# Kernel tuning notes

Hardware: AMD Instinct MI355X
Metric: run time of the kernel (lower is better)

## Reference

```python
import jax, jax.numpy as jnp
import numpy as np

# J6 incidence matrix for Plucker coordinates (constant buffer in the torch module)
_J6 = jnp.array([[0, 0, 0, 0, 0, 1],
                 [0, 0, 0, 0, -1, 0],
                 [0, 0, 0, 1, 0, 0],
                 [0, 0, 1, 0, 0, 0],
                 [0, -1, 0, 0, 0, 0],
                 [1, 0, 0, 0, 0, 0]], dtype=jnp.float32)

# combinations(range(4), 2) index pairs for the exterior product
_PI = np.array([0, 0, 0, 1, 1, 2])
_PJ = np.array([1, 2, 3, 2, 3, 3])


def plucker_lines(p1, p2):
    # p1, p2: (..., 4) -> normalized Plucker 6-vectors (..., 6)
    lines = p1[..., _PI] * p2[..., _PJ] - p1[..., _PJ] * p2[..., _PI]
    n = jnp.linalg.norm(lines, axis=-1, keepdims=True)
    return lines / jnp.maximum(n, 1e-12)


def setup_inputs() -> dict:
    key = jax.random.key(0)
    ks = jax.random.split(key, 6)
    B, T, D, H = 1, 2048, 1024, 16
    s = D ** -0.5
    x = jax.random.normal(ks[0], (B, T, D), jnp.float32)
    Wqkv = jax.random.normal(ks[1], (D, 3 * D), jnp.float32) * s
    bqkv = jnp.zeros((3 * D,), jnp.float32)
    W1p = jax.random.normal(ks[2], (D, 4 * H), jnp.float32) * s
    W2p = jax.random.normal(ks[3], (D, 4 * H), jnp.float32) * s
    plucker_scale = jnp.full((H,), 0.1, jnp.float32)
    Wout = jax.random.normal(ks[4], (D, D), jnp.float32) * s
    bout = jnp.zeros((D,), jnp.float32)
    return {"x": x, "Wqkv": Wqkv, "bqkv": bqkv, "W1p": W1p, "W2p": W2p,
            "plucker_scale": plucker_scale, "Wout": Wout, "bout": bout}


def reference(x, Wqkv, bqkv, W1p, W2p, plucker_scale, Wout, bout):
    B, T, D = x.shape
    H = plucker_scale.shape[0]
    dh = D // H

    qkv = (x @ Wqkv + bqkv).reshape(B, T, 3, H, dh)
    q = jnp.transpose(qkv[:, :, 0], (0, 2, 1, 3))  # [B,H,T,dh]
    k = jnp.transpose(qkv[:, :, 1], (0, 2, 1, 3))
    v = jnp.transpose(qkv[:, :, 2], (0, 2, 1, 3))

    std_logits = jnp.einsum('bhid,bhjd->bhij', q, k) * (dh ** -0.5)

    p1 = (x @ W1p).reshape(B, T, H, 4)
    p2 = (x @ W2p).reshape(B, T, H, 4)
    lines_h = jnp.transpose(plucker_lines(p1, p2), (0, 2, 1, 3))  # [B,H,T,6]
    Jlines = lines_h @ _J6.T                                       # [B,H,T,6]
    plucker_bias = jnp.einsum('bhic,bhjc->bhij', lines_h, Jlines)  # [B,H,T,T]

    logits = std_logits + plucker_bias * plucker_scale[None, :, None, None]
    causal = jnp.triu(jnp.ones((T, T), bool), 1)
    logits = jnp.where(causal[None, None], -jnp.inf, logits)
    attn = jax.nn.softmax(logits, axis=-1)

    out = jnp.einsum('bhij,bhjd->bhid', attn, v)
    out = jnp.transpose(out, (0, 2, 1, 3)).reshape(B, T, D)
    return out @ Wout + bout
```

## Files before the change

kernel.cpp:

```cpp
#include <hip/hip_runtime.h>

typedef unsigned short u16;
typedef unsigned int u32;
typedef __attribute__((ext_vector_type(8))) __bf16 bf16x8;
typedef __attribute__((ext_vector_type(4))) float f32x4;
typedef __attribute__((ext_vector_type(4))) u16 u16x4;

#define MFMA16(a, b, c) __builtin_amdgcn_mfma_f32_16x16x32_bf16((a), (b), (c), 0, 0, 0)

static __device__ __forceinline__ u16 f2b(float f) {
  union { float f; u32 u; } v; v.f = f;
  u32 u = v.u;
  return (u16)((u + 0x7FFFu + ((u >> 16) & 1u)) >> 16);
}

static __device__ __forceinline__ u32 pack2(float a, float b) {
  u32 r;
  asm("v_cvt_pk_bf16_f32 %0, %1, %2" : "=v"(r) : "v"(a), "v"(b));
  return r;
}

static __device__ __forceinline__ float exp2fast(float x) {
#if defined(__has_builtin) && __has_builtin(__builtin_amdgcn_exp2f)
  return __builtin_amdgcn_exp2f(x);
#else
  return __expf(x * 0.6931471805599453f);
#endif
}

static __device__ __forceinline__ void gload16(const u16* gp, u16* lp) {
  __builtin_amdgcn_global_load_lds((__attribute__((address_space(1))) void*)(u16*)gp,
                                   (__attribute__((address_space(3))) void*)lp, 16, 0, 0);
}

__global__ __launch_bounds__(256) void k_prep(const float* __restrict__ Wqkv, const float* __restrict__ Wout,
                                              const float* __restrict__ W1p, const float* __restrict__ W2p,
                                              const float* __restrict__ x,
                                              u16* __restrict__ WB, u16* __restrict__ WoT,
                                              u16* __restrict__ xb) {
  const int b = blockIdx.x;
  const int t = threadIdx.x;
  if (b < 1024) {
    __shared__ float tile[64][65];
    const float* src; u16* dst; int N, n0, k0;
    if (b < 768) { src = Wqkv; dst = WB;  N = 3072; n0 = (b % 48) * 64; k0 = (b / 48) * 64; }
    else { const int bb = b - 768; src = Wout; dst = WoT; N = 1024; n0 = (bb & 15) * 64; k0 = (bb >> 4) * 64; }
    const int rr = t >> 4, cc = (t & 15) << 2;
#pragma unroll
    for (int i = 0; i < 4; ++i) {
      const float4 v = *(const float4*)(src + (size_t)(k0 + rr + i * 16) * N + n0 + cc);
      tile[rr + i * 16][cc + 0] = v.x; tile[rr + i * 16][cc + 1] = v.y;
      tile[rr + i * 16][cc + 2] = v.z; tile[rr + i * 16][cc + 3] = v.w;
    }
    __syncthreads();
    const int nr = t >> 3, kc = (t & 7) << 3;
#pragma unroll
    for (int i = 0; i < 2; ++i) {
      u16 o[8];
#pragma unroll
      for (int j = 0; j < 8; ++j) o[j] = f2b(tile[kc + j][nr + i * 32]);
      *(uint4*)(dst + (size_t)(n0 + nr + i * 32) * 1024 + k0 + kc) = *(const uint4*)o;
    }
  } else if (b < 1536) {
    const int idx = (b - 1024) * 256 + t;
    const int j = idx >> 10, k = idx & 1023;
    const float v = (j < 64) ? W1p[(size_t)k * 64 + j] : W2p[(size_t)k * 64 + (j - 64)];
    WB[(size_t)3072 * 1024 + idx] = f2b(v);
  } else {
    const size_t idx = ((size_t)(b - 1536) * 256 + t) << 2;
    const float4 v = *(const float4*)(x + idx);
    u16x4 o; o.x = f2b(v.x); o.y = f2b(v.y); o.z = f2b(v.z); o.w = f2b(v.w);
    *(u16x4*)(xb + idx) = o;
  }
}

static __device__ __forceinline__ void gemm_core_128x64(const u16* __restrict__ A, const u16* __restrict__ B,
                                                        int brow, int bcol, int K,
                                                        u16* ldsA, u16* ldsB, f32x4 acc[4][2]) {
  const int tid = threadIdx.x;
  const int wave = tid >> 6, lane = tid & 63;
  const int wr = wave >> 1, wc = wave & 1;
  const int g = lane >> 4, l15 = lane & 15;

  for (int k0 = 0; k0 < K; k0 += 64) {
#pragma unroll
    for (int li = 0; li < 4; ++li) {
      const int f = li * 256 + wave * 64 + lane;
      const int row = f >> 3;
      const int slot = f & 7;
      const int gcol = ((slot ^ (row & 7)) << 3);
      gload16(A + (size_t)(brow + row) * K + k0 + gcol, ldsA + (size_t)(li * 256 + wave * 64) * 8);
    }
#pragma unroll
    for (int li = 0; li < 2; ++li) {
      const int f = li * 256 + wave * 64 + lane;
      const int row = f >> 3;
      const int slot = f & 7;
      const int gcol = ((slot ^ (row & 7)) << 3);
      gload16(B + (size_t)(bcol + row) * K + k0 + gcol, ldsB + (size_t)(li * 256 + wave * 64) * 8);
    }
    __syncthreads();
    bf16x8 af[4][2], bfr[2][2];
#pragma unroll
    for (int kk = 0; kk < 2; ++kk) {
#pragma unroll
      for (int m = 0; m < 4; ++m) {
        const int rowA = wr * 64 + m * 16 + l15;
        const int chA = (kk * 4 + g) ^ (rowA & 7);
        af[m][kk] = *(const bf16x8*)(ldsA + (size_t)rowA * 64 + chA * 8);
      }
#pragma unroll
      for (int n = 0; n < 2; ++n) {
        const int rowB = wc * 32 + n * 16 + l15;
        const int chB = (kk * 4 + g) ^ (rowB & 7);
        bfr[n][kk] = *(const bf16x8*)(ldsB + (size_t)rowB * 64 + chB * 8);
      }
    }
#pragma unroll
    for (int m = 0; m < 4; ++m)
#pragma unroll
      for (int n = 0; n < 2; ++n)
#pragma unroll
        for (int kk = 0; kk < 2; ++kk)
          acc[m][n] = MFMA16(af[m][kk], bfr[n][kk], acc[m][n]);
    __syncthreads();
  }
}

__global__ __launch_bounds__(256) void k_gemm_qkvp(const u16* __restrict__ xb, const u16* __restrict__ WB,
                                                   const float* __restrict__ bqkv,
                                                   u16* __restrict__ Qext, u16* __restrict__ Kext,
                                                   u16* __restrict__ Vt, float* __restrict__ P12) {
  __shared__ __align__(16) u16 ldsA[128 * 64];
  __shared__ __align__(16) u16 ldsB[64 * 64];
  const int bid = blockIdx.x;
  const int bn = bid % 50, bm = bid / 50;
  f32x4 acc[4][2];
#pragma unroll
  for (int m = 0; m < 4; ++m)
#pragma unroll
    for (int n = 0; n < 2; ++n) acc[m][n] = (f32x4){0.f, 0.f, 0.f, 0.f};
  gemm_core_128x64(xb, WB, bm * 128, bn * 64, 1024, ldsA, ldsB, acc);

  const int tid = threadIdx.x;
  const int wave = tid >> 6, lane = tid & 63;
  const int wr = wave >> 1, wc = wave & 1;
  const int g = lane >> 4, l15 = lane & 15;
  const int tbase = bm * 128 + wr * 64 + g * 4;
  const int cbase = bn * 64 + wc * 32 + l15;
#pragma unroll
  for (int m = 0; m < 4; ++m) {
#pragma unroll
    for (int n = 0; n < 2; ++n) {
      const int c = cbase + n * 16;
#pragma unroll
      for (int r = 0; r < 4; ++r) {
        const int t = tbase + m * 16 + r;
        float v = acc[m][n][r];
        if (c < 3072) {
          v += bqkv[c];
          const int sub = c >> 10;
          const int rem = c & 1023;
          const int hh = rem >> 6, d = rem & 63;
          if (sub == 0)      Qext[((size_t)hh * 2048 + t) * 96 + d] = f2b(v * 0.18033688f);
          else if (sub == 1) Kext[((size_t)hh * 2048 + t) * 96 + d] = f2b(v);
          else               Vt[(size_t)hh * 131072 + (size_t)(t >> 5) * 2048 + d * 32 + (t & 31)] = f2b(v);
        } else {
          P12[(size_t)t * 128 + (c - 3072)] = v;
        }
      }
    }
  }
}

__global__ __launch_bounds__(256) void k_lines(const float* __restrict__ P12, const float* __restrict__ pscale,
                                               u16* __restrict__ Qext, u16* __restrict__ Kext) {
  const int idx = blockIdx.x * 256 + threadIdx.x;
  const int t = idx >> 4, h = idx & 15;
  const float* p = P12 + (size_t)t * 128;
  const float a0 = p[h * 4 + 0], a1 = p[h * 4 + 1], a2 = p[h * 4 + 2], a3 = p[h * 4 + 3];
  const float b0 = p[64 + h * 4 + 0], b1 = p[64 + h * 4 + 1], b2 = p[64 + h * 4 + 2], b3 = p[64 + h * 4 + 3];
  float L0 = a0 * b1 - a1 * b0;
  float L1 = a0 * b2 - a2 * b0;
  float L2 = a0 * b3 - a3 * b0;
  float L3 = a1 * b2 - a2 * b1;
  float L4 = a1 * b3 - a3 * b1;
  float L5 = a2 * b3 - a3 * b2;
  const float nrm = sqrtf(L0 * L0 + L1 * L1 + L2 * L2 + L3 * L3 + L4 * L4 + L5 * L5);
  const float inv = 1.0f / fmaxf(nrm, 1e-12f);
  L0 *= inv; L1 *= inv; L2 *= inv; L3 *= inv; L4 *= inv; L5 *= inv;
  const float s = pscale[h] * 1.44269504f;
  u16* q = Qext + ((size_t)h * 2048 + t) * 96 + 64;
  u16* k = Kext + ((size_t)h * 2048 + t) * 96 + 64;
  q[0] = f2b(L0 * s); q[1] = f2b(L1 * s); q[2] = f2b(L2 * s);
  q[3] = f2b(L3 * s); q[4] = f2b(L4 * s); q[5] = f2b(L5 * s);
  k[0] = f2b(L5); k[1] = f2b(-L4); k[2] = f2b(L3);
  k[3] = f2b(L2); k[4] = f2b(-L1); k[5] = f2b(L0);
#pragma unroll
  for (int c = 6; c < 32; ++c) { q[c] = 0; k[c] = 0; }
}

__global__ __launch_bounds__(128) void k_attn(const u16* __restrict__ Qext, const u16* __restrict__ Kext,
                                              const u16* __restrict__ Vt, u16* __restrict__ AO) {
  const int bid = blockIdx.x;
  const int h = bid & 15;
  const int p = ((bid >> 4) << 1) + (threadIdx.x >> 6);
  const int lane = threadIdx.x & 63;
  const int g = lane >> 4, l15 = lane & 15;
  const int q0A = p << 4;
  const int q0B = (127 - p) << 4;
  const int qgA = q0A + l15;
  const int qgB = q0B + l15;
  const int sA = (p >> 1) + 1;
  const int sB = ((127 - p) >> 1) + 1;
  const u16* Qh = Qext + (size_t)h * 2048 * 96;
  const u16* Kh = Kext + (size_t)h * 2048 * 96;
  const u16* Vh = Vt + (size_t)h * 131072;

  bf16x8 aqA[3], aqB[3];
#pragma unroll
  for (int ks = 0; ks < 3; ++ks) {
    aqA[ks] = *(const bf16x8*)(Qh + (size_t)qgA * 96 + ks * 32 + g * 8);
    aqB[ks] = *(const bf16x8*)(Qh + (size_t)qgB * 96 + ks * 32 + g * 8);
  }

  f32x4 accA[4], accB[4];
#pragma unroll
  for (int n = 0; n < 4; ++n) {
    accA[n] = (f32x4){0.f, 0.f, 0.f, 0.f};
    accB[n] = (f32x4){0.f, 0.f, 0.f, 0.f};
  }
  float lA = 0.f, lB = 0.f;

  const u16* Kbase = Kh + (size_t)l15 * 96 + g * 8;
  const u16* Vlane = Vh + (size_t)l15 * 32 + g * 8;

  bf16x8 kX0[3], kX1[3], kY0[3], kY1[3];
  bf16x8 avX[4], avY[4];
  f32x4 SA0c, SA1c, SB0c, SB1c, SA0n, SA1n, SB0n, SB1n;

  {
#pragma unroll
    for (int ks = 0; ks < 3; ++ks) {
      kX0[ks] = *(const bf16x8*)(Kbase + ks * 32);
      kX1[ks] = *(const bf16x8*)(Kbase + 16 * 96 + ks * 32);
    }
    SB0c = (f32x4){0.f, 0.f, 0.f, 0.f}; SB1c = SB0c; SA0c = SB0c; SA1c = SB0c;
#pragma unroll
    for (int ks = 0; ks < 3; ++ks) {
      SB0c = MFMA16(kX0[ks], aqB[ks], SB0c);
      SB1c = MFMA16(kX1[ks], aqB[ks], SB1c);
      SA0c = MFMA16(kX0[ks], aqA[ks], SA0c);
      SA1c = MFMA16(kX1[ks], aqA[ks], SA1c);
    }
    const u16* kp = Kbase + (size_t)((1 < sB) ? 1 : 0) * 32 * 96;
#pragma unroll
    for (int ks = 0; ks < 3; ++ks) {
      kY0[ks] = *(const bf16x8*)(kp + ks * 32);
      kY1[ks] = *(const bf16x8*)(kp + 16 * 96 + ks * 32);
    }
#pragma unroll
    for (int n = 0; n < 4; ++n) avX[n] = *(const bf16x8*)(Vlane + n * 512);
  }

#define GLUE(S0, S1, Q0S, QGS, LS, PBS)                                           \
  {                                                                               \
    if (jb + 31 > Q0S) {                                                          \
      _Pragma("unroll")                                                           \
      for (int r = 0; r < 4; ++r) {                                               \
        if (jb + g * 4 + r > QGS) S0[r] = -1e30f;                                 \
        if (jb + 16 + g * 4 + r > QGS) S1[r] = -1e30f;                            \
      }                                                                           \
    }                                                                             \
    _Pragma("unroll")                                                             \
    for (int r = 0; r < 4; ++r) {                                                 \
      S0[r] = exp2fast(S0[r]);                                                    \
      S1[r] = exp2fast(S1[r]);                                                    \
    }                                                                             \
    LS += ((S0[0] + S0[1]) + (S0[2] + S0[3])) + ((S1[0] + S1[1]) + (S1[2] + S1[3])); \
    u32 a0 = pack2(S0[0], S0[1]);                                                 \
    u32 a1 = pack2(S0[2], S0[3]);                                                 \
    u32 b0 = pack2(S1[0], S1[1]);                                                 \
    u32 b1 = pack2(S1[2], S1[3]);                                                 \
    asm("v_permlane32_swap_b32 %0, %1" : "+v"(a0), "+v"(b0));                     \
    asm("v_permlane16_swap_b32 %0, %1" : "+v"(a0), "+v"(b0));                     \
    asm("v_permlane32_swap_b32 %0, %1" : "+v"(a1), "+v"(b1));                     \
    asm("v_permlane16_swap_b32 %0, %1" : "+v"(a1), "+v"(b1));                     \
    PBS.u[0] = a0;                                                                \
    PBS.u[1] = a1;                                                                \
    PBS.u[2] = b0;                                                                \
    PBS.u[3] = b1;                                                                \
  }

#define ATTN_STEP(SA0C, SA1C, SB0C, SB1C, SA0N, SA1N, SB0N, SB1N, KN0, KN1, KL0, KL1, AVC, AVN) \
  {                                                                               \
    const int jb = jt * 32;                                                       \
    const int jn1 = (jt + 1 < sB) ? jt + 1 : jt;                                  \
    const int jn2 = (jt + 2 < sB) ? jt + 2 : jt;                                  \
                                     \
    SB0N = (f32x4){0.f, 0.f, 0.f, 0.f}; SB1N = SB0N;                              \
    __builtin_amdgcn_s_setprio(1);                                                \
    _Pragma("unroll")                                                             \
    for (int ks = 0; ks < 3; ++ks) {                                              \
      SB0N = MFMA16(KN0[ks], aqB[ks], SB0N);                                      \
      SB1N = MFMA16(KN1[ks], aqB[ks], SB1N);                                      \
    }                                                                             \
    if (jt + 1 < sA) {                                                            \
      SA0N = (f32x4){0.f, 0.f, 0.f, 0.f}; SA1N = SA0N;                            \
      _Pragma("unroll")                                                           \
      for (int ks = 0; ks < 3; ++ks) {                                            \
        SA0N = MFMA16(KN0[ks], aqA[ks], SA0N);                                    \
        SA1N = MFMA16(KN1[ks], aqA[ks], SA1N);                                    \
      }                                                                           \
    }                                                                             \
    __builtin_amdgcn_s_setprio(0);                                                \
                                                         \
    const u16* kp = Kbase + (size_t)jn2 * 32 * 96;                                \
    _Pragma("unroll")                                                             \
    for (int ks = 0; ks < 3; ++ks) {                                              \
      KL0[ks] = *(const bf16x8*)(kp + ks * 32);                                   \
      KL1[ks] = *(const bf16x8*)(kp + 16 * 96 + ks * 32);                         \
    }                                                                             \
                                                         \
    _Pragma("unroll")                                                             \
    for (int n = 0; n < 4; ++n)                                                   \
      AVN[n] = *(const bf16x8*)(Vlane + (size_t)jn1 * 2048 + n * 512);            \
                                                      \
    union { u32 u[4]; bf16x8 bv; } pbB, pbA;                                      \
    GLUE(SB0C, SB1C, q0B, qgB, lB, pbB);                                          \
    const bool actA = (jt < sA);                                                  \
    if (actA) GLUE(SA0C, SA1C, q0A, qgA, lA, pbA);                                \
                                                 \
    __builtin_amdgcn_s_setprio(1);                                                \
    _Pragma("unroll")                                                             \
    for (int n = 0; n < 4; ++n) accB[n] = MFMA16(AVC[n], pbB.bv, accB[n]);        \
    if (actA) {                                                                   \
      _Pragma("unroll")                                                           \
      for (int n = 0; n < 4; ++n) accA[n] = MFMA16(AVC[n], pbA.bv, accA[n]);      \
    }                                                                             \
    __builtin_amdgcn_s_setprio(0);                                                \
  }

  int jt = 0;
  for (;;) {
    ATTN_STEP(SA0c, SA1c, SB0c, SB1c, SA0n, SA1n, SB0n, SB1n, kY0, kY1, kX0, kX1, avX, avY);
    if (++jt >= sB) break;
    ATTN_STEP(SA0n, SA1n, SB0n, SB1n, SA0c, SA1c, SB0c, SB1c, kX0, kX1, kY0, kY1, avY, avX);
    if (++jt >= sB) break;
  }
#undef ATTN_STEP
#undef GLUE

  lA += __shfl_xor(lA, 16);
  lA += __shfl_xor(lA, 32);
  lB += __shfl_xor(lB, 16);
  lB += __shfl_xor(lB, 32);
  const float invA = 1.0f / lA;
  const float invB = 1.0f / lB;
  u32* dstA = (u32*)(AO + (size_t)qgA * 1024 + h * 64 + g * 4);
  u32* dstB = (u32*)(AO + (size_t)qgB * 1024 + h * 64 + g * 4);
#pragma unroll
  for (int n = 0; n < 4; ++n) {
    dstA[n * 8 + 0] = pack2(accA[n][0] * invA, accA[n][1] * invA);
    dstA[n * 8 + 1] = pack2(accA[n][2] * invA, accA[n][3] * invA);
    dstB[n * 8 + 0] = pack2(accB[n][0] * invB, accB[n][1] * invB);
    dstB[n * 8 + 1] = pack2(accB[n][2] * invB, accB[n][3] * invB);
  }
}

__global__ __launch_bounds__(256) void k_gemm_out(const u16* __restrict__ AO, const u16* __restrict__ WoT,
                                                  const float* __restrict__ bout, float* __restrict__ out) {
  __shared__ __align__(16) u16 ldsA[128 * 64];
  __shared__ __align__(16) u16 ldsB[32 * 64];
  const int bid = blockIdx.x;
  const int bn = bid & 31, bm = bid >> 5;
  const int tid = threadIdx.x;
  const int wave = tid >> 6, lane = tid & 63;
  const int wr = wave >> 1, wc = wave & 1;
  const int g = lane >> 4, l15 = lane & 15;

  f32x4 acc[4];
#pragma unroll
  for (int m = 0; m < 4; ++m) acc[m] = (f32x4){0.f, 0.f, 0.f, 0.f};

  for (int k0 = 0; k0 < 1024; k0 += 64) {
#pragma unroll
    for (int li = 0; li < 4; ++li) {
      const int f = li * 256 + wave * 64 + lane;
      const int row = f >> 3;
      const int slot = f & 7;
      const int gcol = ((slot ^ (row & 7)) << 3);
      gload16(AO + (size_t)(bm * 128 + row) * 1024 + k0 + gcol, ldsA + (size_t)(li * 256 + wave * 64) * 8);
    }
    {
      const int f = wave * 64 + lane;
      const int row = f >> 3;
      const int slot = f & 7;
      const int gcol = ((slot ^ (row & 7)) << 3);
      gload16(WoT + (size_t)(bn * 32 + row) * 1024 + k0 + gcol, ldsB + (size_t)(wave * 64) * 8);
    }
    __syncthreads();
    bf16x8 af[4][2], bfr[2];
#pragma unroll
    for (int kk = 0; kk < 2; ++kk) {
#pragma unroll
      for (int m = 0; m < 4; ++m) {
        const int rowA = wr * 64 + m * 16 + l15;
        const int chA = (kk * 4 + g) ^ (rowA & 7);
        af[m][kk] = *(const bf16x8*)(ldsA + (size_t)rowA * 64 + chA * 8);
      }
      const int rowB = wc * 16 + l15;
      const int chB = (kk * 4 + g) ^ (rowB & 7);
      bfr[kk] = *(const bf16x8*)(ldsB + (size_t)rowB * 64 + chB * 8);
    }
#pragma unroll
    for (int m = 0; m < 4; ++m)
#pragma unroll
      for (int kk = 0; kk < 2; ++kk)
        acc[m] = MFMA16(af[m][kk], bfr[kk], acc[m]);
    __syncthreads();
  }

  const int tbase = bm * 128 + wr * 64 + g * 4;
  const int c = bn * 32 + wc * 16 + l15;
  const float bb = bout[c];
#pragma unroll
  for (int m = 0; m < 4; ++m)
#pragma unroll
    for (int r = 0; r < 4; ++r) {
      const int t = tbase + m * 16 + r;
      out[(size_t)t * 1024 + c] = acc[m][r] + bb;
    }
}

extern "C" void kernel_launch(void* const* d_in, const int* in_sizes, int n_in,
                              void* d_out, int out_size, void* d_ws, size_t ws_size,
                              hipStream_t stream) {
  const float* x      = (const float*)d_in[0];
  const float* Wqkv   = (const float*)d_in[1];
  const float* bqkv   = (const float*)d_in[2];
  const float* W1p    = (const float*)d_in[3];
  const float* W2p    = (const float*)d_in[4];
  const float* pscale = (const float*)d_in[5];
  const float* Wout   = (const float*)d_in[6];
  const float* bout   = (const float*)d_in[7];
  float* out = (float*)d_out;

  char* ws = (char*)d_ws;
  u16*   WB    = (u16*)(ws + 0);
  u16*   WoT   = (u16*)(ws + 6553600);
  u16*   xb    = (u16*)(ws + 8650752);
  u16*   Qext  = (u16*)(ws + 12845056);
  u16*   Kext  = (u16*)(ws + 19136512);
  u16*   Vt    = (u16*)(ws + 25427968);
  float* P12   = (float*)(ws + 29622272);
  u16*   AO    = (u16*)(ws + 30670848);

  k_prep<<<3584, 256, 0, stream>>>(Wqkv, Wout, W1p, W2p, x, WB, WoT, xb);
  k_gemm_qkvp<<<800, 256, 0, stream>>>(xb, WB, bqkv, Qext, Kext, Vt, P12);
  k_lines<<<128, 256, 0, stream>>>(P12, pscale, Qext, Kext);
  k_attn<<<512, 128, 0, stream>>>(Qext, Kext, Vt, AO);
  k_gemm_out<<<512, 256, 0, stream>>>(AO, WoT, bout, out);
}
```

Before: 98.92 us.

## Share K/V tiles across four waves via double-buffered LDS in attention

Attention blocks now hold four waves covering 64 consecutive queries of one head. They cooperatively stage each 32-key K/V tile into a double-buffered LDS region, instead of every wave streaming K/V from global memory on its own. K is written by the QKV GEMM and the lines kernel in a pre-swizzled MFMA-fragment layout, so each stage is a contiguous copy and each wave reads its fragment with one vector load per chunk. This cuts redundant global/L2 K/V traffic. In exchange it drops the old two-query-tile interleaving that balanced causal work and hid latency, and adds a block barrier per key tile, where waves with shorter causal ranges sit idle.

```diff
diff --git a/kernel.cpp b/kernel.cpp
--- a/kernel.cpp
+++ b/kernel.cpp
@@ -129,7 +129,7 @@
 
 __global__ __launch_bounds__(256) void k_gemm_qkvp(const u16* __restrict__ xb, const u16* __restrict__ WB,
                                                    const float* __restrict__ bqkv,
-                                                   u16* __restrict__ Qext, u16* __restrict__ Kext,
+                                                   u16* __restrict__ Qext, u16* __restrict__ Kf,
                                                    u16* __restrict__ Vt, float* __restrict__ P12) {
   __shared__ __align__(16) u16 ldsA[128 * 64];
   __shared__ __align__(16) u16 ldsB[64 * 64];
@@ -162,9 +162,15 @@
           const int sub = c >> 10;
           const int rem = c & 1023;
           const int hh = rem >> 6, d = rem & 63;
-          if (sub == 0)      Qext[((size_t)hh * 2048 + t) * 96 + d] = f2b(v * 0.18033688f);
-          else if (sub == 1) Kext[((size_t)hh * 2048 + t) * 96 + d] = f2b(v);
-          else               Vt[(size_t)hh * 131072 + (size_t)(t >> 5) * 2048 + d * 32 + (t & 31)] = f2b(v);
+          if (sub == 0) {
+            Qext[((size_t)hh * 2048 + t) * 96 + d] = f2b(v * 0.18033688f);
+          } else if (sub == 1) {
+            const int jt2 = t >> 5, hf = (t >> 4) & 1, l15t = t & 15;
+            const int ks2 = d >> 5, gg = (d >> 3) & 3, e = d & 7;
+            Kf[(size_t)hh * 196608 + (size_t)jt2 * 3072 + (hf * 3 + ks2) * 512 + (gg * 16 + l15t) * 8 + e] = f2b(v);
+          } else {
+            Vt[(size_t)hh * 131072 + (size_t)(t >> 5) * 2048 + d * 32 + (t & 31)] = f2b(v);
+          }
         } else {
           P12[(size_t)t * 128 + (c - 3072)] = v;
         }
@@ -174,7 +180,7 @@
 }
 
 __global__ __launch_bounds__(256) void k_lines(const float* __restrict__ P12, const float* __restrict__ pscale,
-                                               u16* __restrict__ Qext, u16* __restrict__ Kext) {
+                                               u16* __restrict__ Qext, u16* __restrict__ Kf) {
   const int idx = blockIdx.x * 256 + threadIdx.x;
   const int t = idx >> 4, h = idx & 15;
   const float* p = P12 + (size_t)t * 128;
@@ -191,180 +197,129 @@
   L0 *= inv; L1 *= inv; L2 *= inv; L3 *= inv; L4 *= inv; L5 *= inv;
   const float s = pscale[h] * 1.44269504f;
   u16* q = Qext + ((size_t)h * 2048 + t) * 96 + 64;
-  u16* k = Kext + ((size_t)h * 2048 + t) * 96 + 64;
   q[0] = f2b(L0 * s); q[1] = f2b(L1 * s); q[2] = f2b(L2 * s);
   q[3] = f2b(L3 * s); q[4] = f2b(L4 * s); q[5] = f2b(L5 * s);
-  k[0] = f2b(L5); k[1] = f2b(-L4); k[2] = f2b(L3);
-  k[3] = f2b(L2); k[4] = f2b(-L1); k[5] = f2b(L0);
-#pragma unroll
-  for (int c = 6; c < 32; ++c) { q[c] = 0; k[c] = 0; }
-}
-
-__global__ __launch_bounds__(128) void k_attn(const u16* __restrict__ Qext, const u16* __restrict__ Kext,
+#pragma unroll
+  for (int c = 6; c < 32; ++c) q[c] = 0;
+  const float kv0 = L5, kv1 = -L4, kv2 = L3, kv3 = L2, kv4 = -L1, kv5 = L0;
+  const int jt = t >> 5, hf = (t >> 4) & 1, l15t = t & 15;
+  u16* kf = Kf + (size_t)h * 196608 + (size_t)jt * 3072 + (hf * 3 + 2) * 512;
+#pragma unroll
+  for (int j = 0; j < 32; ++j) {
+    const int gg = (j >> 3) & 3, e = j & 7;
+    float val;
+    if (j == 0) val = kv0; else if (j == 1) val = kv1; else if (j == 2) val = kv2;
+    else if (j == 3) val = kv3; else if (j == 4) val = kv4; else if (j == 5) val = kv5;
+    else val = 0.f;
+    kf[(gg * 16 + l15t) * 8 + e] = (j < 6) ? f2b(val) : (u16)0;
+  }
+}
+
+__global__ __launch_bounds__(256) void k_attn(const u16* __restrict__ Qext, const u16* __restrict__ Kf,
                                               const u16* __restrict__ Vt, u16* __restrict__ AO) {
-  const int bid = blockIdx.x;
-  const int h = bid & 15;
-  const int p = ((bid >> 4) << 1) + (threadIdx.x >> 6);
-  const int lane = threadIdx.x & 63;
+  __shared__ __align__(16) u16 KV[2][5120];
+  const int idx = blockIdx.x;
+  const int half = idx >> 8;
+  const int qt_raw = (idx & 255) >> 4;
+  const int qt = half ? (31 - qt_raw) : qt_raw;
+  const int h = idx & 15;
+  const int wave = threadIdx.x >> 6, lane = threadIdx.x & 63;
   const int g = lane >> 4, l15 = lane & 15;
-  const int q0A = p << 4;
-  const int q0B = (127 - p) << 4;
-  const int qgA = q0A + l15;
-  const int qgB = q0B + l15;
-  const int sA = (p >> 1) + 1;
-  const int sB = ((127 - p) >> 1) + 1;
+  const int q0 = qt * 64 + wave * 16;
+  const int q_glob = q0 + l15;
+  const int sW = (q0 >> 5) + 1;
+  const int sBlk = qt * 2 + 2;
   const u16* Qh = Qext + (size_t)h * 2048 * 96;
-  const u16* Kh = Kext + (size_t)h * 2048 * 96;
-  const u16* Vh = Vt + (size_t)h * 131072;
-
-  bf16x8 aqA[3], aqB[3];
-#pragma unroll
-  for (int ks = 0; ks < 3; ++ks) {
-    aqA[ks] = *(const bf16x8*)(Qh + (size_t)qgA * 96 + ks * 32 + g * 8);
-    aqB[ks] = *(const bf16x8*)(Qh + (size_t)qgB * 96 + ks * 32 + g * 8);
-  }
-
-  f32x4 accA[4], accB[4];
+  const u16* Ktiles = Kf + (size_t)h * 196608;
+  const u16* Vtiles = Vt + (size_t)h * 131072;
+
+  bf16x8 aq[3];
+#pragma unroll
+  for (int ks = 0; ks < 3; ++ks)
+    aq[ks] = *(const bf16x8*)(Qh + (size_t)q_glob * 96 + ks * 32 + g * 8);
+
+  f32x4 accO[4];
+#pragma unroll
+  for (int n = 0; n < 4; ++n) accO[n] = (f32x4){0.f, 0.f, 0.f, 0.f};
+  float lrun = 0.f;
+
+#define STAGE(JT, B)                                                              \
+  {                                                                               \
+    const u16* ksrc = Ktiles + (size_t)(JT) * 3072;                               \
+    const u16* vsrc = Vtiles + (size_t)(JT) * 2048;                               \
+    u16* kb = &KV[B][0];                                                          \
+    u16* vb = &KV[B][3072];                                                       \
+    gload16(ksrc + (wave * 64 + lane) * 8, kb + wave * 512);                      \
+    if (wave < 2) gload16(ksrc + ((wave + 4) * 64 + lane) * 8, kb + (wave + 4) * 512); \
+    else          gload16(vsrc + ((wave - 2) * 64 + lane) * 8, vb + (wave - 2) * 512); \
+    if (wave < 2) gload16(vsrc + ((wave + 2) * 64 + lane) * 8, vb + (wave + 2) * 512); \
+  }
+
+  STAGE(0, 0);
+  __syncthreads();
+
+  int cur = 0;
+  for (int jt = 0; jt < sBlk; ++jt) {
+    if (jt + 1 < sBlk) STAGE(jt + 1, cur ^ 1);
+    if (jt < sW) {
+      const u16* kb = &KV[cur][0];
+      const u16* vb = &KV[cur][3072];
+      bf16x8 kc[6];
+#pragma unroll
+      for (int z = 0; z < 6; ++z) kc[z] = *(const bf16x8*)(kb + z * 512 + lane * 8);
+      bf16x8 av[4];
+#pragma unroll
+      for (int n = 0; n < 4; ++n) av[n] = *(const bf16x8*)(vb + (n * 16 + l15) * 32 + g * 8);
+      f32x4 S0 = (f32x4){0.f, 0.f, 0.f, 0.f}, S1 = (f32x4){0.f, 0.f, 0.f, 0.f};
+      __builtin_amdgcn_s_setprio(1);
+#pragma unroll
+      for (int ks = 0; ks < 3; ++ks) {
+        S0 = MFMA16(kc[ks], aq[ks], S0);
+        S1 = MFMA16(kc[3 + ks], aq[ks], S1);
+      }
+      __builtin_amdgcn_s_setprio(0);
+      const int jb = jt * 32;
+      if (jb + 31 > q0) {
+#pragma unroll
+        for (int r = 0; r < 4; ++r) {
+          if (jb + g * 4 + r > q_glob) S0[r] = -1e30f;
+          if (jb + 16 + g * 4 + r > q_glob) S1[r] = -1e30f;
+        }
+      }
+#pragma unroll
+      for (int r = 0; r < 4; ++r) {
+        S0[r] = exp2fast(S0[r]);
+        S1[r] = exp2fast(S1[r]);
+      }
+      lrun += ((S0[0] + S0[1]) + (S0[2] + S0[3])) + ((S1[0] + S1[1]) + (S1[2] + S1[3]));
+      u32 a0 = pack2(S0[0], S0[1]);
+      u32 a1 = pack2(S0[2], S0[3]);
+      u32 b0 = pack2(S1[0], S1[1]);
+      u32 b1 = pack2(S1[2], S1[3]);
+      asm("v_permlane32_swap_b32 %0, %1" : "+v"(a0), "+v"(b0));
+      asm("v_permlane16_swap_b32 %0, %1" : "+v"(a0), "+v"(b0));
+      asm("v_permlane32_swap_b32 %0, %1" : "+v"(a1), "+v"(b1));
+      asm("v_permlane16_swap_b32 %0, %1" : "+v"(a1), "+v"(b1));
+      union { u32 u[4]; bf16x8 bv; } pb;
+      pb.u[0] = a0; pb.u[1] = a1; pb.u[2] = b0; pb.u[3] = b1;
+      __builtin_amdgcn_s_setprio(1);
+#pragma unroll
+      for (int n = 0; n < 4; ++n) accO[n] = MFMA16(av[n], pb.bv, accO[n]);
+      __builtin_amdgcn_s_setprio(0);
+    }
+    __syncthreads();
+    cur ^= 1;
+  }
+#undef STAGE
+
+  lrun += __shfl_xor(lrun, 16);
+  lrun += __shfl_xor(lrun, 32);
+  const float inv = 1.0f / lrun;
+  u32* dst = (u32*)(AO + (size_t)q_glob * 1024 + h * 64 + g * 4);
 #pragma unroll
   for (int n = 0; n < 4; ++n) {
-    accA[n] = (f32x4){0.f, 0.f, 0.f, 0.f};
-    accB[n] = (f32x4){0.f, 0.f, 0.f, 0.f};
-  }
-  float lA = 0.f, lB = 0.f;
-
-  const u16* Kbase = Kh + (size_t)l15 * 96 + g * 8;
-  const u16* Vlane = Vh + (size_t)l15 * 32 + g * 8;
-
-  bf16x8 kX0[3], kX1[3], kY0[3], kY1[3];
-  bf16x8 avX[4], avY[4];
-  f32x4 SA0c, SA1c, SB0c, SB1c, SA0n, SA1n, SB0n, SB1n;
-
-  {
-#pragma unroll
-    for (int ks = 0; ks < 3; ++ks) {
-      kX0[ks] = *(const bf16x8*)(Kbase + ks * 32);
-      kX1[ks] = *(const bf16x8*)(Kbase + 16 * 96 + ks * 32);
-    }
-    SB0c = (f32x4){0.f, 0.f, 0.f, 0.f}; SB1c = SB0c; SA0c = SB0c; SA1c = SB0c;
-#pragma unroll
-    for (int ks = 0; ks < 3; ++ks) {
-      SB0c = MFMA16(kX0[ks], aqB[ks], SB0c);
-      SB1c = MFMA16(kX1[ks], aqB[ks], SB1c);
-      SA0c = MFMA16(kX0[ks], aqA[ks], SA0c);
-      SA1c = MFMA16(kX1[ks], aqA[ks], SA1c);
-    }
-    const u16* kp = Kbase + (size_t)((1 < sB) ? 1 : 0) * 32 * 96;
-#pragma unroll
-    for (int ks = 0; ks < 3; ++ks) {
-      kY0[ks] = *(const bf16x8*)(kp + ks * 32);
-      kY1[ks] = *(const bf16x8*)(kp + 16 * 96 + ks * 32);
-    }
-#pragma unroll
-    for (int n = 0; n < 4; ++n) avX[n] = *(const bf16x8*)(Vlane + n * 512);
-  }
-
-#define GLUE(S0, S1, Q0S, QGS, LS, PBS)                                           \
-  {                                                                               \
-    if (jb + 31 > Q0S) {                                                          \
-      _Pragma("unroll")                                                           \
-      for (int r = 0; r < 4; ++r) {                                               \
-        if (jb + g * 4 + r > QGS) S0[r] = -1e30f;                                 \
-        if (jb + 16 + g * 4 + r > QGS) S1[r] = -1e30f;                            \
-      }                                                                           \
-    }                                                                             \
-    _Pragma("unroll")                                                             \
-    for (int r = 0; r < 4; ++r) {                                                 \
-      S0[r] = exp2fast(S0[r]);                                                    \
-      S1[r] = exp2fast(S1[r]);                                                    \
-    }                                                                             \
-    LS += ((S0[0] + S0[1]) + (S0[2] + S0[3])) + ((S1[0] + S1[1]) + (S1[2] + S1[3])); \
-    u32 a0 = pack2(S0[0], S0[1]);                                                 \
-    u32 a1 = pack2(S0[2], S0[3]);                                                 \
-    u32 b0 = pack2(S1[0], S1[1]);                                                 \
-    u32 b1 = pack2(S1[2], S1[3]);                                                 \
-    asm("v_permlane32_swap_b32 %0, %1" : "+v"(a0), "+v"(b0));                     \
-    asm("v_permlane16_swap_b32 %0, %1" : "+v"(a0), "+v"(b0));                     \
-    asm("v_permlane32_swap_b32 %0, %1" : "+v"(a1), "+v"(b1));                     \
-    asm("v_permlane16_swap_b32 %0, %1" : "+v"(a1), "+v"(b1));                     \
-    PBS.u[0] = a0;                                                                \
-    PBS.u[1] = a1;                                                                \
-    PBS.u[2] = b0;                                                                \
-    PBS.u[3] = b1;                                                                \
-  }
-
-#define ATTN_STEP(SA0C, SA1C, SB0C, SB1C, SA0N, SA1N, SB0N, SB1N, KN0, KN1, KL0, KL1, AVC, AVN) \
-  {                                                                               \
-    const int jb = jt * 32;                                                       \
-    const int jn1 = (jt + 1 < sB) ? jt + 1 : jt;                                  \
-    const int jn2 = (jt + 2 < sB) ? jt + 2 : jt;                                  \
-                                     \
-    SB0N = (f32x4){0.f, 0.f, 0.f, 0.f}; SB1N = SB0N;                              \
-    __builtin_amdgcn_s_setprio(1);                                                \
-    _Pragma("unroll")                                                             \
-    for (int ks = 0; ks < 3; ++ks) {                                              \
-      SB0N = MFMA16(KN0[ks], aqB[ks], SB0N);                                      \
-      SB1N = MFMA16(KN1[ks], aqB[ks], SB1N);                                      \
-    }                                                                             \
-    if (jt + 1 < sA) {                                                            \
-      SA0N = (f32x4){0.f, 0.f, 0.f, 0.f}; SA1N = SA0N;                            \
-      _Pragma("unroll")                                                           \
-      for (int ks = 0; ks < 3; ++ks) {                                            \
-        SA0N = MFMA16(KN0[ks], aqA[ks], SA0N);                                    \
-        SA1N = MFMA16(KN1[ks], aqA[ks], SA1N);                                    \
-      }                                                                           \
-    }                                                                             \
-    __builtin_amdgcn_s_setprio(0);                                                \
-                                                         \
-    const u16* kp = Kbase + (size_t)jn2 * 32 * 96;                                \
-    _Pragma("unroll")                                                             \
-    for (int ks = 0; ks < 3; ++ks) {                                              \
-      KL0[ks] = *(const bf16x8*)(kp + ks * 32);                                   \
-      KL1[ks] = *(const bf16x8*)(kp + 16 * 96 + ks * 32);                         \
-    }                                                                             \
-                                                         \
-    _Pragma("unroll")                                                             \
-    for (int n = 0; n < 4; ++n)                                                   \
-      AVN[n] = *(const bf16x8*)(Vlane + (size_t)jn1 * 2048 + n * 512);            \
-                                                      \
-    union { u32 u[4]; bf16x8 bv; } pbB, pbA;                                      \
-    GLUE(SB0C, SB1C, q0B, qgB, lB, pbB);                                          \
-    const bool actA = (jt < sA);                                                  \
-    if (actA) GLUE(SA0C, SA1C, q0A, qgA, lA, pbA);                                \
-                                                 \
-    __builtin_amdgcn_s_setprio(1);                                                \
-    _Pragma("unroll")                                                             \
-    for (int n = 0; n < 4; ++n) accB[n] = MFMA16(AVC[n], pbB.bv, accB[n]);        \
-    if (actA) {                                                                   \
-      _Pragma("unroll")                                                           \
-      for (int n = 0; n < 4; ++n) accA[n] = MFMA16(AVC[n], pbA.bv, accA[n]);      \
-    }                                                                             \
-    __builtin_amdgcn_s_setprio(0);                                                \
-  }
-
-  int jt = 0;
-  for (;;) {
-    ATTN_STEP(SA0c, SA1c, SB0c, SB1c, SA0n, SA1n, SB0n, SB1n, kY0, kY1, kX0, kX1, avX, avY);
-    if (++jt >= sB) break;
-    ATTN_STEP(SA0n, SA1n, SB0n, SB1n, SA0c, SA1c, SB0c, SB1c, kX0, kX1, kY0, kY1, avY, avX);
-    if (++jt >= sB) break;
-  }
-#undef ATTN_STEP
-#undef GLUE
-
-  lA += __shfl_xor(lA, 16);
-  lA += __shfl_xor(lA, 32);
-  lB += __shfl_xor(lB, 16);
-  lB += __shfl_xor(lB, 32);
-  const float invA = 1.0f / lA;
-  const float invB = 1.0f / lB;
-  u32* dstA = (u32*)(AO + (size_t)qgA * 1024 + h * 64 + g * 4);
-  u32* dstB = (u32*)(AO + (size_t)qgB * 1024 + h * 64 + g * 4);
-#pragma unroll
-  for (int n = 0; n < 4; ++n) {
-    dstA[n * 8 + 0] = pack2(accA[n][0] * invA, accA[n][1] * invA);
-    dstA[n * 8 + 1] = pack2(accA[n][2] * invA, accA[n][3] * invA);
-    dstB[n * 8 + 0] = pack2(accB[n][0] * invB, accB[n][1] * invB);
-    dstB[n * 8 + 1] = pack2(accB[n][2] * invB, accB[n][3] * invB);
+    dst[n * 8 + 0] = pack2(accO[n][0] * inv, accO[n][1] * inv);
+    dst[n * 8 + 1] = pack2(accO[n][2] * inv, accO[n][3] * inv);
   }
 }
 
@@ -451,14 +406,14 @@
   u16*   WoT   = (u16*)(ws + 6553600);
   u16*   xb    = (u16*)(ws + 8650752);
   u16*   Qext  = (u16*)(ws + 12845056);
-  u16*   Kext  = (u16*)(ws + 19136512);
+  u16*   Kf    = (u16*)(ws + 19136512);
   u16*   Vt    = (u16*)(ws + 25427968);
   float* P12   = (float*)(ws + 29622272);
   u16*   AO    = (u16*)(ws + 30670848);
 
   k_prep<<<3584, 256, 0, stream>>>(Wqkv, Wout, W1p, W2p, x, WB, WoT, xb);
-  k_gemm_qkvp<<<800, 256, 0, stream>>>(xb, WB, bqkv, Qext, Kext, Vt, P12);
-  k_lines<<<128, 256, 0, stream>>>(P12, pscale, Qext, Kext);
-  k_attn<<<512, 128, 0, stream>>>(Qext, Kext, Vt, AO);
+  k_gemm_qkvp<<<800, 256, 0, stream>>>(xb, WB, bqkv, Qext, Kf, Vt, P12);
+  k_lines<<<128, 256, 0, stream>>>(P12, pscale, Qext, Kf);
+  k_attn<<<512, 256, 0, stream>>>(Qext, Kf, Vt, AO);
   k_gemm_out<<<512, 256, 0, stream>>>(AO, WoT, bout, out);
 }
```

Measured after the change: 103.1 us. 1.04x slower.
